# Kernel optimization log

Hardware: AMD Instinct MI355X
Metric: run time of the kernel (lower is better)

## Reference

```python
import jax, jax.numpy as jnp
import numpy as np

N = 50000      # num vertices
M = 10000      # num hyperedges
NNZ = 1600000  # incidence list length (avg degree 32)
D = 128        # in_features == out_features


def setup_inputs() -> dict:
    key = jax.random.key(0)
    k0, k1, k2, k3, k4, k5 = jax.random.split(key, 6)
    X = jax.random.normal(k0, (N, D), dtype=jnp.float32)
    X0 = jax.random.normal(k1, (N, D), dtype=jnp.float32)
    vertex = jax.random.randint(k2, (NNZ,), 0, N)
    edges = jax.random.randint(k3, (NNZ,), 0, M)
    # nn.Linear(D, D, bias=False) weight, kaiming-uniform-ish scale
    W = jax.random.uniform(k4, (D, D), dtype=jnp.float32,
                           minval=-1.0, maxval=1.0) / np.float32(np.sqrt(D))
    alpha = jax.random.uniform(k5, (), dtype=jnp.float32)
    beta = jnp.float32(0.5)
    return {"X": X, "X0": X0, "W": W, "alpha": alpha, "beta": beta,
            "vertex": vertex, "edges": edges}


def _scatter_mean(vals, idx, num_segments):
    # segment mean; empty segments -> 0 (matches torch_scatter 'mean')
    s = jax.ops.segment_sum(vals, idx, num_segments=num_segments)
    cnt = jax.ops.segment_sum(jnp.ones(idx.shape, vals.dtype), idx,
                              num_segments=num_segments)
    return s / jnp.maximum(cnt, 1.0)[:, None]


def reference(X, X0, W, alpha, beta, vertex, edges):
    Xve = X[vertex]                          # [NNZ, D] gather vertex -> incidence
    Xe = _scatter_mean(Xve, edges, M)        # [M, D]   hyperedge features
    Xev = Xe[edges]                          # [NNZ, D] gather edge -> incidence
    Xv = _scatter_mean(Xev, vertex, N)       # [N, D]   back to vertices
    Xi = (1.0 - alpha) * Xv + alpha * X0     # initial-residual mix
    return (1.0 - beta) * Xi + beta * (Xi @ W.T)  # identity-map mix + linear
```

## Files before the change

kernel.cpp:

```cpp
#include <hip/hip_runtime.h>
#include <hip/hip_bf16.h>


#define DD 128
#define NV 50000
#define ME 10000

#define CHUNK 2048
#define NEB 157
#define NVB 196
#define CAP_E 12288
#define CAP_V 9728

typedef __hip_bfloat16 bf16;
typedef __attribute__((ext_vector_type(8))) short short8v;
typedef __attribute__((ext_vector_type(4))) float float4v;
typedef __attribute__((ext_vector_type(4))) unsigned uint4v;

#define OFF_XE    0
#define OFF_ELIST 2560000
#define OFF_VLIST 8960000
#define OFF_EPV   15360000
#define OFF_EPK   19218432
#define OFF_VPV   21147648
#define OFF_VPK   24961024
#define OFF_XB    15360000
#define OFF_VOFF  28160000
#define OFF_EOFF  28360064
#define OFF_ECUR  28400128
#define OFF_VCUR  28400756
#define OFF_GBE   28401664
#define OFF_GBV   28402304
#define OFF_FLAG  28404608
#define OFF_WF    28404624
#define WS_USED   28470160

__device__ __forceinline__ float bf2f(unsigned short s) {
    union { unsigned u; float f; } x; x.u = ((unsigned)s) << 16; return x.f;
}
__device__ __forceinline__ unsigned f2bfu(float x) {
    union { bf16 h; unsigned short u; } c; c.h = __float2bfloat16(x); return (unsigned)c.u;
}
__device__ __forceinline__ float loadf(const void* p, long long i, unsigned f32) {
    if (f32) return ((const float*)p)[i];
    return bf2f(((const unsigned short*)p)[i]);
}
__device__ __forceinline__ float u2f_lo(unsigned x) {
    union { unsigned u; float f; } c; c.u = x << 16; return c.f;
}
__device__ __forceinline__ float u2f_hi(unsigned x) {
    union { unsigned u; float f; } c; c.u = x & 0xFFFF0000u; return c.f;
}
__device__ __forceinline__ void acc8(const uint4& u, float* a) {
    a[0] += u2f_lo(u.x); a[1] += u2f_hi(u.x);
    a[2] += u2f_lo(u.y); a[3] += u2f_hi(u.y);
    a[4] += u2f_lo(u.z); a[5] += u2f_hi(u.z);
    a[6] += u2f_lo(u.w); a[7] += u2f_hi(u.w);
}

__device__ __forceinline__ unsigned wave_iscan(unsigned x, int lane) {
#pragma unroll
    for (int s = 1; s < 64; s <<= 1) {
        unsigned u = __shfl_up(x, s);
        if (lane >= s) x += u;
    }
    return x;
}

__device__ __forceinline__ unsigned wave_is_fp32(const unsigned short* p) {
    int l = threadIdx.x & 63;
    int big = 0;
    for (int i = l; i < 256; i += 64) {
        unsigned e = (p[i] >> 7) & 0xFFu;
        if (e >= 0x90u) big++;
    }
    for (int s = 32; s > 0; s >>= 1) big += __shfl_down(big, s);
    return (__shfl(big, 0) >= 4) ? 1u : 0u;
}

__global__ __launch_bounds__(256) void prep_pairs(const void* X, const void* X0, const void* W,
                                                  const void* beta_p,
                                                  const int* __restrict__ vertex,
                                                  const int* __restrict__ edges,
                                                  unsigned* __restrict__ flags,
                                                  unsigned short* __restrict__ Wfrag,
                                                  unsigned* __restrict__ ecur,
                                                  unsigned* __restrict__ vcur,
                                                  unsigned short* __restrict__ epval,
                                                  unsigned char* __restrict__ epkey,
                                                  unsigned short* __restrict__ vpval,
                                                  unsigned char* __restrict__ vpkey,
                                                  int nchunks, int nnz) {
    __shared__ unsigned buf[CHUNK];
    __shared__ unsigned hist[256];
    __shared__ unsigned loff[256], cur[256], gbase[256];
    __shared__ unsigned wsum[4];
    int b = blockIdx.x, t = threadIdx.x;

    if (b == 0) {
        if (t < 64) {
            const unsigned short* px[3] = {(const unsigned short*)X,
                                           (const unsigned short*)X0,
                                           (const unsigned short*)W};
            for (int k = 0; k < 3; k++) {
                int big = 0;
                for (int i = t; i < 256; i += 64) {
                    unsigned e = (px[k][i] >> 7) & 0xFFu;
                    if (e >= 0x90u) big++;
                }
                for (int s = 32; s > 0; s >>= 1) big += __shfl_down(big, s);
                if (t == 0) flags[k] = (big >= 4) ? 1u : 0u;
            }
            if (t == 0) {
                unsigned short bb = *(const unsigned short*)beta_p;
                flags[3] = (bb == 0x3F00u) ? 0u : 1u;
            }
        }
        return;
    }

    if (b <= 8) {
        int blob = (b - 1) * 256 + t;
        unsigned fW = wave_is_fp32((const unsigned short*)W);
        unsigned short bu = *(const unsigned short*)beta_p;
        unsigned fS = (bu == 0x3F00u) ? 0u : 1u;
        int lane = blob & 63, kk = (blob >> 6) & 3, ct = blob >> 8;
        int nn = lane & 15, quad = lane >> 4;
        int c = ct * 16 + nn;
        int kbase = kk * 32 + quad * 8;
        float beta = loadf(beta_p, 0, fS);
        float omb = 1.f - beta;
        unsigned short hi[8], lo[8];
#pragma unroll
        for (int j = 0; j < 8; j++) {
            float wv = loadf(W, (long long)c * DD + kbase + j, fW);
            float v = beta * wv + ((kbase + j) == c ? omb : 0.f);
            unsigned short hh = (unsigned short)f2bfu(v);
            hi[j] = hh;
            lo[j] = (unsigned short)f2bfu(v - bf2f(hh));
        }
        uint4 ph, pl;
        ph.x = (unsigned)hi[0] | ((unsigned)hi[1] << 16);
        ph.y = (unsigned)hi[2] | ((unsigned)hi[3] << 16);
        ph.z = (unsigned)hi[4] | ((unsigned)hi[5] << 16);
        ph.w = (unsigned)hi[6] | ((unsigned)hi[7] << 16);
        pl.x = (unsigned)lo[0] | ((unsigned)lo[1] << 16);
        pl.y = (unsigned)lo[2] | ((unsigned)lo[3] << 16);
        pl.z = (unsigned)lo[4] | ((unsigned)lo[5] << 16);
        pl.w = (unsigned)lo[6] | ((unsigned)lo[7] << 16);
        ((uint4*)Wfrag)[blob] = ph;
        ((uint4*)Wfrag)[2048 + blob] = pl;
        return;
    }

    int pb = b - 9;
    int side = (pb >= nchunks);
    int chunk = side ? pb - nchunks : pb;
    int base = chunk * CHUNK;
    int len = min(CHUNK, nnz - base);
    if (len <= 0) return;

    int lane = t & 63, w = t >> 6;
    int sh = side ? 24 : 22;
    int nb = side ? NVB : NEB;
    unsigned cap = side ? CAP_V : CAP_E;
    unsigned kmask = side ? 255u : 63u;
    unsigned* curg = side ? vcur : ecur;
    unsigned short* pval = side ? vpval : epval;
    unsigned char* pkey = side ? vpkey : epkey;

    unsigned pkr[8];

    hist[t] = 0;
    __syncthreads();
#pragma unroll
    for (int it = 0; it < 8; it++) {
        int i = t + it * 256;
        if (i < len) {
            unsigned e = (unsigned)edges[base + i];
            unsigned v = (unsigned)vertex[base + i];
            unsigned pk = side ? ((v << 16) | e) : ((e << 16) | v);
            pkr[it] = pk;
            atomicAdd(&hist[pk >> sh], 1u);
        }
    }
    __syncthreads();

    unsigned hv = hist[t];
    unsigned inc = wave_iscan(hv, lane);
    if (lane == 63) wsum[w] = inc;
    __syncthreads();
    if (t == 0) { unsigned a = 0; for (int i = 0; i < 4; i++) { unsigned x = wsum[i]; wsum[i] = a; a += x; } }
    __syncthreads();
    inc += wsum[w];
    unsigned excl = inc - hv;
    loff[t] = excl; cur[t] = excl;
    if (t < nb && hv > 0)
        gbase[t] = t * cap + atomicAdd(&curg[t], hv);
    __syncthreads();

#pragma unroll
    for (int it = 0; it < 8; it++) {
        int i = t + it * 256;
        if (i < len) {
            unsigned pk = pkr[it];
            buf[atomicAdd(&cur[pk >> sh], 1u)] = pk;
        }
    }
    __syncthreads();
    for (int i = t; i < len; i += 256) {
        unsigned pk = buf[i];
        unsigned bb = pk >> sh;
        unsigned pos = gbase[bb] + (i - loff[bb]);
        if (pos < (bb + 1) * cap) {
            pval[pos] = (unsigned short)(pk & 0xFFFFu);
            pkey[pos] = (unsigned char)((pk >> 16) & kmask);
        }
    }
}

__global__ __launch_bounds__(256) void conv_x(const void* __restrict__ X,
                                              unsigned short* __restrict__ Xb,
                                              const unsigned* __restrict__ flags) {
    if (!flags[0]) return;
    int i = blockIdx.x * 256 + threadIdx.x;
    if (i >= NV * DD / 8) return;
    const float4* p = (const float4*)X + (size_t)i * 2;
    float4 a = p[0], b = p[1];
    uint4 o;
    o.x = f2bfu(a.x) | (f2bfu(a.y) << 16);
    o.y = f2bfu(a.z) | (f2bfu(a.w) << 16);
    o.z = f2bfu(b.x) | (f2bfu(b.y) << 16);
    o.w = f2bfu(b.z) | (f2bfu(b.w) << 16);
    ((uint4*)Xb)[i] = o;
}

__global__ void scan353(const unsigned* __restrict__ ecur, const unsigned* __restrict__ vcur,
                        unsigned* __restrict__ gbe, unsigned* __restrict__ gbv,
                        unsigned* __restrict__ voff, unsigned* __restrict__ eoff,
                        int nnz) {
    __shared__ unsigned wsum[8];
    int t = threadIdx.x;
    int lane = t & 63, w = t >> 6;
    unsigned v = 0;
    if (t < NEB) v = ecur[t];
    else if (t < NEB + NVB) v = vcur[t - NEB];
    unsigned inc = wave_iscan(v, lane);
    if (lane == 63) wsum[w] = inc;
    __syncthreads();
    if (t == 0) {
        unsigned a = 0;
        for (int i = 0; i < 8; i++) { unsigned x = wsum[i]; wsum[i] = a; a += x; }
    }
    __syncthreads();
    inc += wsum[w];
    unsigned excl = inc - v;
    if (t < NEB) {
        gbe[t] = excl;
    } else if (t < NEB + NVB) {
        gbv[t - NEB] = excl - (unsigned)nnz;
    }
    if (t == 0) {
        gbe[NEB] = (unsigned)nnz;
        gbv[NVB] = (unsigned)nnz;
        eoff[ME] = (unsigned)nnz;
        voff[NV] = (unsigned)nnz;
    }
}

__global__ __launch_bounds__(256) void build_lists(const unsigned short* __restrict__ epval,
                                                   const unsigned char* __restrict__ epkey,
                                                   const unsigned short* __restrict__ vpval,
                                                   const unsigned char* __restrict__ vpkey,
                                                   const unsigned* __restrict__ gbe,
                                                   const unsigned* __restrict__ gbv,
                                                   unsigned* __restrict__ eoff,
                                                   unsigned* __restrict__ voff,
                                                   unsigned short* __restrict__ elist,
                                                   unsigned short* __restrict__ vlist) {
    __shared__ unsigned offs[256], curs[256];
    __shared__ unsigned wsum2[4];
    int b = blockIdx.x, t = threadIdx.x;
    int lane = t & 63, w = t >> 6;
    const unsigned short* pval;
    const unsigned char* pkey;
    unsigned* off;
    unsigned short* list;
    unsigned s0, s1, pbase;
    int k0, nk;
    if (b < NEB) {
        pval = epval; pkey = epkey; off = eoff; list = elist;
        k0 = b << 6; nk = min(64, ME - k0);
        s0 = gbe[b]; s1 = gbe[b + 1];
        pbase = (unsigned)b * CAP_E;
    } else {
        int bb = b - NEB;
        pval = vpval; pkey = vpkey; off = voff; list = vlist;
        k0 = bb << 8; nk = min(256, NV - k0);
        s0 = gbv[bb]; s1 = gbv[bb + 1];
        pbase = (unsigned)bb * CAP_V;
    }
    int len = (int)(s1 - s0);

    curs[t] = 0;
    __syncthreads();
    for (int i0 = 0; i0 < len; i0 += 2048) {
        unsigned ks[8];
#pragma unroll
        for (int it = 0; it < 8; it++) {
            int i = i0 + t + it * 256;
            if (i < len) ks[it] = pkey[pbase + i];
        }
#pragma unroll
        for (int it = 0; it < 8; it++) {
            int i = i0 + t + it * 256;
            if (i < len) atomicAdd(&curs[ks[it]], 1u);
        }
    }
    __syncthreads();
    unsigned hv = curs[t];
    unsigned inc = wave_iscan(hv, lane);
    if (lane == 63) wsum2[w] = inc;
    __syncthreads();
    if (t == 0) { unsigned a = 0; for (int i = 0; i < 4; i++) { unsigned x = wsum2[i]; wsum2[i] = a; a += x; } }
    __syncthreads();
    inc += wsum2[w];
    unsigned my_excl = inc - hv;
    offs[t] = s0 + my_excl;
    curs[t] = 0;
    if (t < nk) off[k0 + t] = s0 + my_excl;
    __syncthreads();

    for (int i0 = 0; i0 < len; i0 += 2048) {
        unsigned ks[8], vs[8];
#pragma unroll
        for (int it = 0; it < 8; it++) {
            int i = i0 + t + it * 256;
            if (i < len) { ks[it] = pkey[pbase + i]; vs[it] = pval[pbase + i]; }
        }
#pragma unroll
        for (int it = 0; it < 8; it++) {
            int i = i0 + t + it * 256;
            if (i < len) {
                unsigned p = offs[ks[it]] + atomicAdd(&curs[ks[it]], 1u);
                list[p] = (unsigned short)vs[it];
            }
        }
    }
}

__global__ __launch_bounds__(256, 8) void edge_agg(const void* __restrict__ X,
                                                   const unsigned short* __restrict__ Xb,
                                                   const unsigned* __restrict__ eoff,
                                                   const unsigned short* __restrict__ elist,
                                                   unsigned short* __restrict__ Xe,
                                                   const unsigned* __restrict__ flags, int m) {
    __shared__ float red[4][DD];
    int e = blockIdx.x;
    int t = threadIdx.x, lane = t & 63, w = t >> 6;
    const unsigned short* Xp = flags[0] ? Xb : (const unsigned short*)X;
    unsigned s0 = eoff[e], s1 = eoff[e + 1];
    float a[8];
#pragma unroll
    for (int i = 0; i < 8; i++) a[i] = 0.f;

    int sub = t & 15;
    unsigned q = s0 + (unsigned)(t >> 4);
    for (; q + 48 < s1; q += 64) {
        unsigned v0 = __builtin_nontemporal_load(elist + q);
        unsigned v1 = __builtin_nontemporal_load(elist + q + 16);
        unsigned v2 = __builtin_nontemporal_load(elist + q + 32);
        unsigned v3 = __builtin_nontemporal_load(elist + q + 48);
        uint4 u0 = *(const uint4*)(Xp + (size_t)v0 * DD + 8 * sub);
        uint4 u1 = *(const uint4*)(Xp + (size_t)v1 * DD + 8 * sub);
        uint4 u2 = *(const uint4*)(Xp + (size_t)v2 * DD + 8 * sub);
        uint4 u3 = *(const uint4*)(Xp + (size_t)v3 * DD + 8 * sub);
        acc8(u0, a); acc8(u1, a); acc8(u2, a); acc8(u3, a);
    }
    for (; q + 16 < s1; q += 32) {
        unsigned v0 = __builtin_nontemporal_load(elist + q);
        unsigned v1 = __builtin_nontemporal_load(elist + q + 16);
        uint4 u0 = *(const uint4*)(Xp + (size_t)v0 * DD + 8 * sub);
        uint4 u1 = *(const uint4*)(Xp + (size_t)v1 * DD + 8 * sub);
        acc8(u0, a); acc8(u1, a);
    }
    if (q < s1) {
        unsigned v0 = __builtin_nontemporal_load(elist + q);
        uint4 u0 = *(const uint4*)(Xp + (size_t)v0 * DD + 8 * sub);
        acc8(u0, a);
    }
#pragma unroll
    for (int i = 0; i < 8; i++) {
        a[i] += __shfl_xor(a[i], 16);
        a[i] += __shfl_xor(a[i], 32);
    }
    if ((lane >> 4) == 0) {
#pragma unroll
        for (int i = 0; i < 8; i++) red[w][8 * sub + i] = a[i];
    }
    __syncthreads();
    if (t < DD) {
        float inv = (s1 > s0) ? 1.f / (float)(s1 - s0) : 1.f;
        float v = (red[0][t] + red[1][t] + red[2][t] + red[3][t]) * inv;
        Xe[(size_t)e * DD + t] = (unsigned short)f2bfu(v);
    }
}

__global__ __launch_bounds__(256, 6) void vertex_out(const unsigned short* __restrict__ Xe,
                                                     const unsigned* __restrict__ voff,
                                                     const unsigned short* __restrict__ vlist,
                                                     const void* __restrict__ X0,
                                                     const unsigned short* __restrict__ Wfrag,
                                                     const void* __restrict__ alpha_p,
                                                     void* __restrict__ out,
                                                     const unsigned* __restrict__ flags, int n) {
    __shared__ short8v A_hi[272];
    __shared__ short8v A_lo[272];
    __shared__ float x0s[2048];
    __shared__ unsigned short vidx[1024];
    __shared__ unsigned voffs[17];
    int t = threadIdx.x, lane = t & 63, w = t >> 6;
    unsigned fX = flags[0], f0 = flags[1], fS = flags[3];
    float alpha = loadf(alpha_p, 0, fS);
    float oma = 1.f - alpha;
    int v0 = blockIdx.x * 16;
    int nv = min(16, n - v0);

    if (t <= 16) voffs[t] = voff[min(v0 + t, n)];
    __syncthreads();
    unsigned sBase = voffs[0];
    int tot = (int)(voffs[16] - sBase);
    bool staged = tot <= 1024;

    if (staged) {
        for (int i = t; i < tot; i += 256)
            vidx[i] = __builtin_nontemporal_load(vlist + sBase + i);
    }
    if (!f0) {
        int cnt = nv * 16;
        const uint4v* P = (const uint4v*)((const unsigned short*)X0 + (size_t)v0 * DD);
        for (int i = t; i < cnt; i += 256) {
            uint4v u = __builtin_nontemporal_load(P + i);
            float* d = &x0s[i * 8];
            d[0] = u2f_lo(u.x); d[1] = u2f_hi(u.x);
            d[2] = u2f_lo(u.y); d[3] = u2f_hi(u.y);
            d[4] = u2f_lo(u.z); d[5] = u2f_hi(u.z);
            d[6] = u2f_lo(u.w); d[7] = u2f_hi(u.w);
        }
    } else {
        int cnt = nv * 32;
        const float4v* P = (const float4v*)((const float*)X0 + (size_t)v0 * DD);
        for (int i = t; i < cnt; i += 256) {
            float4v u = __builtin_nontemporal_load(P + i);
            *((float4v*)&x0s[i * 4]) = u;
        }
    }
    __syncthreads();

    int g = lane >> 4, sub = lane & 15;
    for (int j = 0; j < 4; j++) {
        int r = w * 4 + j, v = v0 + r;
        int idx = (sub >> 2) * 68 + (sub & 3) * 17 + r;
        float a[8];
#pragma unroll
        for (int i = 0; i < 8; i++) a[i] = 0.f;
        if (v < n) {
            unsigned ls0 = voffs[r] - sBase, ls1 = voffs[r + 1] - sBase;
            unsigned q = ls0;
            if (staged) {
                for (; q + 16 <= ls1; q += 16) {
                    unsigned e0 = vidx[q + g], e1 = vidx[q + 4 + g];
                    unsigned e2 = vidx[q + 8 + g], e3 = vidx[q + 12 + g];
                    uint4 u0 = *(const uint4*)(Xe + (size_t)e0 * DD + 8 * sub);
                    uint4 u1 = *(const uint4*)(Xe + (size_t)e1 * DD + 8 * sub);
                    uint4 u2 = *(const uint4*)(Xe + (size_t)e2 * DD + 8 * sub);
                    uint4 u3 = *(const uint4*)(Xe + (size_t)e3 * DD + 8 * sub);
                    acc8(u0, a); acc8(u1, a); acc8(u2, a); acc8(u3, a);
                }
                for (; q + 4 <= ls1; q += 4) {
                    unsigned e0 = vidx[q + g];
                    uint4 u0 = *(const uint4*)(Xe + (size_t)e0 * DD + 8 * sub);
                    acc8(u0, a);
                }
                if (g < (int)(ls1 - q)) {
                    unsigned e0 = vidx[q + g];
                    uint4 u0 = *(const uint4*)(Xe + (size_t)e0 * DD + 8 * sub);
                    acc8(u0, a);
                }
            } else {
                const unsigned short* vp = vlist + sBase;
                for (; q + 8 <= ls1; q += 8) {
                    unsigned e0 = __builtin_nontemporal_load(vp + q + g);
                    unsigned e1 = __builtin_nontemporal_load(vp + q + 4 + g);
                    uint4 u0 = *(const uint4*)(Xe + (size_t)e0 * DD + 8 * sub);
                    uint4 u1 = *(const uint4*)(Xe + (size_t)e1 * DD + 8 * sub);
                    acc8(u0, a); acc8(u1, a);
                }
                for (; q + 4 <= ls1; q += 4) {
                    unsigned e0 = __builtin_nontemporal_load(vp + q + g);
                    uint4 u0 = *(const uint4*)(Xe + (size_t)e0 * DD + 8 * sub);
                    acc8(u0, a);
                }
                if (g < (int)(ls1 - q)) {
                    unsigned e0 = __builtin_nontemporal_load(vp + q + g);
                    uint4 u0 = *(const uint4*)(Xe + (size_t)e0 * DD + 8 * sub);
                    acc8(u0, a);
                }
            }
#pragma unroll
            for (int i = 0; i < 8; i++) {
                a[i] += __shfl_xor(a[i], 16);
                a[i] += __shfl_xor(a[i], 32);
            }
            if (g == 0) {
                unsigned deg = ls1 - ls0;
                float inv = deg ? 1.f / (float)deg : 1.f;
                const float* xr = &x0s[r * 128 + 8 * sub];
                short8v ah, al;
#pragma unroll
                for (int i = 0; i < 8; i++) {
                    float xi = oma * (a[i] * inv) + alpha * xr[i];
                    unsigned short hh = (unsigned short)f2bfu(xi);
                    ah[i] = (short)hh;
                    al[i] = (short)f2bfu(xi - bf2f(hh));
                }
                A_hi[idx] = ah;
                A_lo[idx] = al;
            }
        } else if (g == 0) {
            short8v zf = {0, 0, 0, 0, 0, 0, 0, 0};
            A_hi[idx] = zf;
            A_lo[idx] = zf;
        }
    }

    __syncthreads();
    int ct = w;
    short8v ah[4], al[4];
#pragma unroll
    for (int kk = 0; kk < 4; kk++) {
        int ridx = kk * 68 + (lane >> 4) * 17 + (lane & 15);
        ah[kk] = A_hi[ridx];
        al[kk] = A_lo[ridx];
    }
    const short8v* Bh = (const short8v*)Wfrag;
    const short8v* Bl = Bh + 2048;
#pragma unroll
    for (int tt = 0; tt < 2; tt++) {
        int c2 = ct + 4 * tt;
        float4v acc = {0.f, 0.f, 0.f, 0.f};
#pragma unroll
        for (int kk = 0; kk < 4; kk++) {
            short8v bh = Bh[(c2 * 4 + kk) * 64 + lane];
            short8v bl = Bl[(c2 * 4 + kk) * 64 + lane];
            acc = __builtin_amdgcn_mfma_f32_16x16x32_bf16(ah[kk], bh, acc, 0, 0, 0);
            acc = __builtin_amdgcn_mfma_f32_16x16x32_bf16(al[kk], bh, acc, 0, 0, 0);
            acc = __builtin_amdgcn_mfma_f32_16x16x32_bf16(ah[kk], bl, acc, 0, 0, 0);
        }
        int col = c2 * 16 + (lane & 15);
        int rbase = v0 + (lane >> 4) * 4;
#pragma unroll
        for (int reg = 0; reg < 4; reg++) {
            int row = rbase + reg;
            if (row < n) {
                if (fX) {
                    __builtin_nontemporal_store(acc[reg],
                        (float*)out + (size_t)row * DD + col);
                } else {
                    bf16 hv = __float2bfloat16(acc[reg]);
                    unsigned short hb = *(unsigned short*)&hv;
                    __builtin_nontemporal_store(hb,
                        (unsigned short*)out + (size_t)row * DD + col);
                }
            }
        }
    }
}

extern "C" void kernel_launch(void* const* d_in, const int* in_sizes, int n_in,
                              void* d_out, int out_size, void* d_ws, size_t ws_size,
                              hipStream_t stream) {
    const void* X      = d_in[0];
    const void* X0     = d_in[1];
    const void* W      = d_in[2];
    const void* alpha  = d_in[3];
    const void* beta   = d_in[4];
    const int*  vertex = (const int*)d_in[5];
    const int*  edges  = (const int*)d_in[6];
    const int nnz = in_sizes[5];

    char* ws = (char*)d_ws;
    unsigned short* Xe = (unsigned short*)(ws + OFF_XE);
    unsigned short* elist = (unsigned short*)(ws + OFF_ELIST);
    unsigned short* vlist = (unsigned short*)(ws + OFF_VLIST);
    unsigned short* epval = (unsigned short*)(ws + OFF_EPV);
    unsigned char*  epkey = (unsigned char*)(ws + OFF_EPK);
    unsigned short* vpval = (unsigned short*)(ws + OFF_VPV);
    unsigned char*  vpkey = (unsigned char*)(ws + OFF_VPK);
    unsigned short* Xb = (unsigned short*)(ws + OFF_XB);
    unsigned* voff   = (unsigned*)(ws + OFF_VOFF);
    unsigned* eoff   = (unsigned*)(ws + OFF_EOFF);
    unsigned* ecur   = (unsigned*)(ws + OFF_ECUR);
    unsigned* vcur   = (unsigned*)(ws + OFF_VCUR);
    unsigned* gbe    = (unsigned*)(ws + OFF_GBE);
    unsigned* gbv    = (unsigned*)(ws + OFF_GBV);
    unsigned* flags  = (unsigned*)(ws + OFF_FLAG);
    unsigned short* Wfrag = (unsigned short*)(ws + OFF_WF);

    hipMemsetAsync(ws + OFF_ECUR, 0, 1412, stream);

    int nchunks = (nnz + CHUNK - 1) / CHUNK;
    prep_pairs<<<9 + 2 * nchunks, 256, 0, stream>>>(X, X0, W, beta, vertex, edges,
                                                    flags, Wfrag, ecur, vcur,
                                                    epval, epkey, vpval, vpkey,
                                                    nchunks, nnz);

    scan353<<<1, 512, 0, stream>>>(ecur, vcur, gbe, gbv, voff, eoff, nnz);

    build_lists<<<NEB + NVB, 256, 0, stream>>>(epval, epkey, vpval, vpkey,
                                               gbe, gbv, eoff, voff, elist, vlist);

    conv_x<<<(NV * DD / 8 + 255) / 256, 256, 0, stream>>>(X, Xb, flags);

    edge_agg<<<ME, 256, 0, stream>>>(X, Xb, eoff, elist, Xe, flags, ME);

    vertex_out<<<(NV + 15) / 16, 256, 0, stream>>>(Xe, voff, vlist, X0, Wfrag,
                                                   alpha, d_out, flags, NV);
}
```

Before: 251.1 us.

## Drop scan kernel via per-bucket offsets and fold X conversion into prep

Removes the single-block scan353 kernel. Lists are now indexed by fixed per-bucket capacity offsets (pbase) plus per-segment degree arrays (edeg/vdeg) rather than compacted global offsets. When the workspace is large enough, the fp32-to-bf16 conversion of X moves into the prep_pairs launch as extra blocks writing to a separate buffer, which removes another launch and lets it overlap with pair bucketing. The trade-off is extra degree loads in the consumer kernels and a dependence on workspace size for the fused path.

```diff
diff --git a/kernel.cpp b/kernel.cpp
--- a/kernel.cpp
+++ b/kernel.cpp
@@ -24,16 +24,17 @@
 #define OFF_EPK   19218432
 #define OFF_VPV   21147648
 #define OFF_VPK   24961024
-#define OFF_XB    15360000
+#define OFF_XBOV  15360000
 #define OFF_VOFF  28160000
 #define OFF_EOFF  28360064
 #define OFF_ECUR  28400128
 #define OFF_VCUR  28400756
-#define OFF_GBE   28401664
-#define OFF_GBV   28402304
 #define OFF_FLAG  28404608
 #define OFF_WF    28404624
-#define WS_USED   28470160
+#define OFF_EDEG  28470160
+#define OFF_VDEG  28490160
+#define OFF_XBSEP 28590160
+#define WS_NEED_SEP 41390160u
 
 __device__ __forceinline__ float bf2f(unsigned short s) {
     union { unsigned u; float f; } x; x.u = ((unsigned)s) << 16; return x.f;
@@ -90,6 +91,7 @@
                                                   unsigned char* __restrict__ epkey,
                                                   unsigned short* __restrict__ vpval,
                                                   unsigned char* __restrict__ vpkey,
+                                                  unsigned short* __restrict__ Xb,
                                                   int nchunks, int nnz) {
     __shared__ unsigned buf[CHUNK];
     __shared__ unsigned hist[256];
@@ -153,70 +155,86 @@
         return;
     }
 
-    int pb = b - 9;
-    int side = (pb >= nchunks);
-    int chunk = side ? pb - nchunks : pb;
-    int base = chunk * CHUNK;
-    int len = min(CHUNK, nnz - base);
-    if (len <= 0) return;
-
-    int lane = t & 63, w = t >> 6;
-    int sh = side ? 24 : 22;
-    int nb = side ? NVB : NEB;
-    unsigned cap = side ? CAP_V : CAP_E;
-    unsigned kmask = side ? 255u : 63u;
-    unsigned* curg = side ? vcur : ecur;
-    unsigned short* pval = side ? vpval : epval;
-    unsigned char* pkey = side ? vpkey : epkey;
-
-    unsigned pkr[8];
-
-    hist[t] = 0;
-    __syncthreads();
-#pragma unroll
-    for (int it = 0; it < 8; it++) {
-        int i = t + it * 256;
-        if (i < len) {
-            unsigned e = (unsigned)edges[base + i];
-            unsigned v = (unsigned)vertex[base + i];
-            unsigned pk = side ? ((v << 16) | e) : ((e << 16) | v);
-            pkr[it] = pk;
-            atomicAdd(&hist[pk >> sh], 1u);
-        }
-    }
-    __syncthreads();
-
-    unsigned hv = hist[t];
-    unsigned inc = wave_iscan(hv, lane);
-    if (lane == 63) wsum[w] = inc;
-    __syncthreads();
-    if (t == 0) { unsigned a = 0; for (int i = 0; i < 4; i++) { unsigned x = wsum[i]; wsum[i] = a; a += x; } }
-    __syncthreads();
-    inc += wsum[w];
-    unsigned excl = inc - hv;
-    loff[t] = excl; cur[t] = excl;
-    if (t < nb && hv > 0)
-        gbase[t] = t * cap + atomicAdd(&curg[t], hv);
-    __syncthreads();
-
-#pragma unroll
-    for (int it = 0; it < 8; it++) {
-        int i = t + it * 256;
-        if (i < len) {
-            unsigned pk = pkr[it];
-            buf[atomicAdd(&cur[pk >> sh], 1u)] = pk;
-        }
-    }
-    __syncthreads();
-    for (int i = t; i < len; i += 256) {
-        unsigned pk = buf[i];
-        unsigned bb = pk >> sh;
-        unsigned pos = gbase[bb] + (i - loff[bb]);
-        if (pos < (bb + 1) * cap) {
-            pval[pos] = (unsigned short)(pk & 0xFFFFu);
-            pkey[pos] = (unsigned char)((pk >> 16) & kmask);
-        }
-    }
+    if (b < 9 + 2 * nchunks) {
+        int pb = b - 9;
+        int side = (pb >= nchunks);
+        int chunk = side ? pb - nchunks : pb;
+        int base = chunk * CHUNK;
+        int len = min(CHUNK, nnz - base);
+        if (len <= 0) return;
+
+        int lane = t & 63, w = t >> 6;
+        int sh = side ? 24 : 22;
+        int nb = side ? NVB : NEB;
+        unsigned cap = side ? CAP_V : CAP_E;
+        unsigned kmask = side ? 255u : 63u;
+        unsigned* curg = side ? vcur : ecur;
+        unsigned short* pval = side ? vpval : epval;
+        unsigned char* pkey = side ? vpkey : epkey;
+
+        unsigned pkr[8];
+
+        hist[t] = 0;
+        __syncthreads();
+#pragma unroll
+        for (int it = 0; it < 8; it++) {
+            int i = t + it * 256;
+            if (i < len) {
+                unsigned e = (unsigned)edges[base + i];
+                unsigned v = (unsigned)vertex[base + i];
+                unsigned pk = side ? ((v << 16) | e) : ((e << 16) | v);
+                pkr[it] = pk;
+                atomicAdd(&hist[pk >> sh], 1u);
+            }
+        }
+        __syncthreads();
+
+        unsigned hv = hist[t];
+        unsigned inc = wave_iscan(hv, lane);
+        if (lane == 63) wsum[w] = inc;
+        __syncthreads();
+        if (t == 0) { unsigned a = 0; for (int i = 0; i < 4; i++) { unsigned x = wsum[i]; wsum[i] = a; a += x; } }
+        __syncthreads();
+        inc += wsum[w];
+        unsigned excl = inc - hv;
+        loff[t] = excl; cur[t] = excl;
+        if (t < nb && hv > 0)
+            gbase[t] = t * cap + atomicAdd(&curg[t], hv);
+        __syncthreads();
+
+#pragma unroll
+        for (int it = 0; it < 8; it++) {
+            int i = t + it * 256;
+            if (i < len) {
+                unsigned pk = pkr[it];
+                buf[atomicAdd(&cur[pk >> sh], 1u)] = pk;
+            }
+        }
+        __syncthreads();
+        for (int i = t; i < len; i += 256) {
+            unsigned pk = buf[i];
+            unsigned bb = pk >> sh;
+            unsigned pos = gbase[bb] + (i - loff[bb]);
+            if (pos < (bb + 1) * cap) {
+                pval[pos] = (unsigned short)(pk & 0xFFFFu);
+                pkey[pos] = (unsigned char)((pk >> 16) & kmask);
+            }
+        }
+        return;
+    }
+
+    unsigned fX = wave_is_fp32((const unsigned short*)X);
+    if (!fX) return;
+    int i = (b - 9 - 2 * nchunks) * 256 + t;
+    if (i >= NV * DD / 8) return;
+    const float4* p = (const float4*)X + (size_t)i * 2;
+    float4 a = p[0], bb = p[1];
+    uint4 o;
+    o.x = f2bfu(a.x) | (f2bfu(a.y) << 16);
+    o.y = f2bfu(a.z) | (f2bfu(a.w) << 16);
+    o.z = f2bfu(bb.x) | (f2bfu(bb.y) << 16);
+    o.w = f2bfu(bb.z) | (f2bfu(bb.w) << 16);
+    ((uint4*)Xb)[i] = o;
 }
 
 __global__ __launch_bounds__(256) void conv_x(const void* __restrict__ X,
@@ -235,47 +253,16 @@
     ((uint4*)Xb)[i] = o;
 }
 
-__global__ void scan353(const unsigned* __restrict__ ecur, const unsigned* __restrict__ vcur,
-                        unsigned* __restrict__ gbe, unsigned* __restrict__ gbv,
-                        unsigned* __restrict__ voff, unsigned* __restrict__ eoff,
-                        int nnz) {
-    __shared__ unsigned wsum[8];
-    int t = threadIdx.x;
-    int lane = t & 63, w = t >> 6;
-    unsigned v = 0;
-    if (t < NEB) v = ecur[t];
-    else if (t < NEB + NVB) v = vcur[t - NEB];
-    unsigned inc = wave_iscan(v, lane);
-    if (lane == 63) wsum[w] = inc;
-    __syncthreads();
-    if (t == 0) {
-        unsigned a = 0;
-        for (int i = 0; i < 8; i++) { unsigned x = wsum[i]; wsum[i] = a; a += x; }
-    }
-    __syncthreads();
-    inc += wsum[w];
-    unsigned excl = inc - v;
-    if (t < NEB) {
-        gbe[t] = excl;
-    } else if (t < NEB + NVB) {
-        gbv[t - NEB] = excl - (unsigned)nnz;
-    }
-    if (t == 0) {
-        gbe[NEB] = (unsigned)nnz;
-        gbv[NVB] = (unsigned)nnz;
-        eoff[ME] = (unsigned)nnz;
-        voff[NV] = (unsigned)nnz;
-    }
-}
-
 __global__ __launch_bounds__(256) void build_lists(const unsigned short* __restrict__ epval,
                                                    const unsigned char* __restrict__ epkey,
                                                    const unsigned short* __restrict__ vpval,
                                                    const unsigned char* __restrict__ vpkey,
-                                                   const unsigned* __restrict__ gbe,
-                                                   const unsigned* __restrict__ gbv,
+                                                   const unsigned* __restrict__ ecur,
+                                                   const unsigned* __restrict__ vcur,
                                                    unsigned* __restrict__ eoff,
                                                    unsigned* __restrict__ voff,
+                                                   unsigned short* __restrict__ edeg,
+                                                   unsigned short* __restrict__ vdeg,
                                                    unsigned short* __restrict__ elist,
                                                    unsigned short* __restrict__ vlist) {
     __shared__ unsigned offs[256], curs[256];
@@ -285,22 +272,22 @@
     const unsigned short* pval;
     const unsigned char* pkey;
     unsigned* off;
+    unsigned short* deg;
     unsigned short* list;
-    unsigned s0, s1, pbase;
-    int k0, nk;
+    unsigned pbase;
+    int k0, nk, len;
     if (b < NEB) {
-        pval = epval; pkey = epkey; off = eoff; list = elist;
+        pval = epval; pkey = epkey; off = eoff; deg = edeg; list = elist;
         k0 = b << 6; nk = min(64, ME - k0);
-        s0 = gbe[b]; s1 = gbe[b + 1];
+        len = (int)ecur[b];
         pbase = (unsigned)b * CAP_E;
     } else {
         int bb = b - NEB;
-        pval = vpval; pkey = vpkey; off = voff; list = vlist;
+        pval = vpval; pkey = vpkey; off = voff; deg = vdeg; list = vlist;
         k0 = bb << 8; nk = min(256, NV - k0);
-        s0 = gbv[bb]; s1 = gbv[bb + 1];
+        len = (int)vcur[bb];
         pbase = (unsigned)bb * CAP_V;
     }
-    int len = (int)(s1 - s0);
 
     curs[t] = 0;
     __syncthreads();
@@ -326,9 +313,12 @@
     __syncthreads();
     inc += wsum2[w];
     unsigned my_excl = inc - hv;
-    offs[t] = s0 + my_excl;
+    offs[t] = pbase + my_excl;
     curs[t] = 0;
-    if (t < nk) off[k0 + t] = s0 + my_excl;
+    if (t < nk) {
+        off[k0 + t] = pbase + my_excl;
+        deg[k0 + t] = (unsigned short)hv;
+    }
     __syncthreads();
 
     for (int i0 = 0; i0 < len; i0 += 2048) {
@@ -352,6 +342,7 @@
 __global__ __launch_bounds__(256, 8) void edge_agg(const void* __restrict__ X,
                                                    const unsigned short* __restrict__ Xb,
                                                    const unsigned* __restrict__ eoff,
+                                                   const unsigned short* __restrict__ edeg,
                                                    const unsigned short* __restrict__ elist,
                                                    unsigned short* __restrict__ Xe,
                                                    const unsigned* __restrict__ flags, int m) {
@@ -359,7 +350,9 @@
     int e = blockIdx.x;
     int t = threadIdx.x, lane = t & 63, w = t >> 6;
     const unsigned short* Xp = flags[0] ? Xb : (const unsigned short*)X;
-    unsigned s0 = eoff[e], s1 = eoff[e + 1];
+    unsigned s0 = eoff[e];
+    unsigned dg = edeg[e];
+    unsigned s1 = s0 + dg;
     float a[8];
 #pragma unroll
     for (int i = 0; i < 8; i++) a[i] = 0.f;
@@ -400,7 +393,7 @@
     }
     __syncthreads();
     if (t < DD) {
-        float inv = (s1 > s0) ? 1.f / (float)(s1 - s0) : 1.f;
+        float inv = dg ? 1.f / (float)dg : 1.f;
         float v = (red[0][t] + red[1][t] + red[2][t] + red[3][t]) * inv;
         Xe[(size_t)e * DD + t] = (unsigned short)f2bfu(v);
     }
@@ -408,6 +401,7 @@
 
 __global__ __launch_bounds__(256, 6) void vertex_out(const unsigned short* __restrict__ Xe,
                                                      const unsigned* __restrict__ voff,
+                                                     const unsigned short* __restrict__ vdeg,
                                                      const unsigned short* __restrict__ vlist,
                                                      const void* __restrict__ X0,
                                                      const unsigned short* __restrict__ Wfrag,
@@ -418,7 +412,8 @@
     __shared__ short8v A_lo[272];
     __shared__ float x0s[2048];
     __shared__ unsigned short vidx[1024];
-    __shared__ unsigned voffs[17];
+    __shared__ unsigned voffs[16];
+    __shared__ unsigned short vdegs[16];
     int t = threadIdx.x, lane = t & 63, w = t >> 6;
     unsigned fX = flags[0], f0 = flags[1], fS = flags[3];
     float alpha = loadf(alpha_p, 0, fS);
@@ -426,11 +421,15 @@
     int v0 = blockIdx.x * 16;
     int nv = min(16, n - v0);
 
-    if (t <= 16) voffs[t] = voff[min(v0 + t, n)];
+    if (t < 16) {
+        int vv = min(v0 + t, n - 1);
+        voffs[t] = voff[vv];
+        vdegs[t] = vdeg[vv];
+    }
     __syncthreads();
     unsigned sBase = voffs[0];
-    int tot = (int)(voffs[16] - sBase);
-    bool staged = tot <= 1024;
+    int tot = (int)((voffs[nv - 1] + vdegs[nv - 1]) - sBase);
+    bool staged = tot <= 1024 && tot >= 0;
 
     if (staged) {
         for (int i = t; i < tot; i += 256)
@@ -465,7 +464,9 @@
 #pragma unroll
         for (int i = 0; i < 8; i++) a[i] = 0.f;
         if (v < n) {
-            unsigned ls0 = voffs[r] - sBase, ls1 = voffs[r + 1] - sBase;
+            unsigned ls0 = voffs[r] - sBase;
+            unsigned dg = vdegs[r];
+            unsigned ls1 = ls0 + dg;
             unsigned q = ls0;
             if (staged) {
                 for (; q + 16 <= ls1; q += 16) {
@@ -513,8 +514,7 @@
                 a[i] += __shfl_xor(a[i], 32);
             }
             if (g == 0) {
-                unsigned deg = ls1 - ls0;
-                float inv = deg ? 1.f / (float)deg : 1.f;
+                float inv = dg ? 1.f / (float)dg : 1.f;
                 const float* xr = &x0s[r * 128 + 8 * sub];
                 short8v ah, al;
 #pragma unroll
@@ -597,33 +597,36 @@
     unsigned char*  epkey = (unsigned char*)(ws + OFF_EPK);
     unsigned short* vpval = (unsigned short*)(ws + OFF_VPV);
     unsigned char*  vpkey = (unsigned char*)(ws + OFF_VPK);
-    unsigned short* Xb = (unsigned short*)(ws + OFF_XB);
     unsigned* voff   = (unsigned*)(ws + OFF_VOFF);
     unsigned* eoff   = (unsigned*)(ws + OFF_EOFF);
     unsigned* ecur   = (unsigned*)(ws + OFF_ECUR);
     unsigned* vcur   = (unsigned*)(ws + OFF_VCUR);
-    unsigned* gbe    = (unsigned*)(ws + OFF_GBE);
-    unsigned* gbv    = (unsigned*)(ws + OFF_GBV);
+    unsigned short* edeg = (unsigned short*)(ws + OFF_EDEG);
+    unsigned short* vdeg = (unsigned short*)(ws + OFF_VDEG);
     unsigned* flags  = (unsigned*)(ws + OFF_FLAG);
     unsigned short* Wfrag = (unsigned short*)(ws + OFF_WF);
 
+    bool sep = (ws_size >= (size_t)WS_NEED_SEP);
+    unsigned short* Xb = (unsigned short*)(ws + (sep ? OFF_XBSEP : OFF_XBOV));
+
     hipMemsetAsync(ws + OFF_ECUR, 0, 1412, stream);
 
     int nchunks = (nnz + CHUNK - 1) / CHUNK;
-    prep_pairs<<<9 + 2 * nchunks, 256, 0, stream>>>(X, X0, W, beta, vertex, edges,
-                                                    flags, Wfrag, ecur, vcur,
-                                                    epval, epkey, vpval, vpkey,
-                                                    nchunks, nnz);
-
-    scan353<<<1, 512, 0, stream>>>(ecur, vcur, gbe, gbv, voff, eoff, nnz);
+    int nconv = sep ? 3125 : 0;
+    prep_pairs<<<9 + 2 * nchunks + nconv, 256, 0, stream>>>(
+        X, X0, W, beta, vertex, edges, flags, Wfrag, ecur, vcur,
+        epval, epkey, vpval, vpkey, Xb, nchunks, nnz);
 
     build_lists<<<NEB + NVB, 256, 0, stream>>>(epval, epkey, vpval, vpkey,
-                                               gbe, gbv, eoff, voff, elist, vlist);
-
-    conv_x<<<(NV * DD / 8 + 255) / 256, 256, 0, stream>>>(X, Xb, flags);
-
-    edge_agg<<<ME, 256, 0, stream>>>(X, Xb, eoff, elist, Xe, flags, ME);
-
-    vertex_out<<<(NV + 15) / 16, 256, 0, stream>>>(Xe, voff, vlist, X0, Wfrag,
+                                               ecur, vcur, eoff, voff,
+                                               edeg, vdeg, elist, vlist);
+
+    if (!sep) {
+        conv_x<<<(NV * DD / 8 + 255) / 256, 256, 0, stream>>>(X, Xb, flags);
+    }
+
+    edge_agg<<<ME, 256, 0, stream>>>(X, Xb, eoff, edeg, elist, Xe, flags, ME);
+
+    vertex_out<<<(NV + 15) / 16, 256, 0, stream>>>(Xe, voff, vdeg, vlist, X0, Wfrag,
                                                    alpha, d_out, flags, NV);
 }
```

New measurement: 264.6 us. +5.4%, slower.
